# Optimization experiments

Measured on AMD Instinct MI355X. Metric: run time of the kernel, lower is better.

The kernel has to match this reference:

```python
import jax, jax.numpy as jnp
import numpy as np

HEADS = 16
DIM_HEAD = 64
WINDOW = 128
LOOK_BACKWARD = 1
LOOK_FORWARD = 0
THETA = 10000.0
PAD_VALUE = -1


def look_around(x, backward, forward, pad_value, axis):
    """Gather overlapping windows: concat shifted copies along the intra-window axis."""
    w = x.shape[axis]
    size = backward + forward + 1
    pads = [(0, 0)] * x.ndim
    pads[axis] = (backward, forward)
    p = jnp.pad(x, pads, constant_values=pad_value)
    segs = [jax.lax.slice_in_dim(p, s, s + w, axis=axis) for s in range(size)]
    return jnp.concatenate(segs, axis=axis + 1)


def rotate_half(t):
    t1, t2 = jnp.split(t, 2, axis=-1)
    return jnp.concatenate([-t2, t1], axis=-1)


def setup_inputs() -> dict:
    key = jax.random.key(0)
    k1, k2, k3 = jax.random.split(key, 3)
    dim = 1024
    x = jax.random.normal(k1, (4, 4096, dim), dtype=jnp.float32)
    W_qkv = jax.random.normal(k2, (dim, 3 * HEADS * DIM_HEAD), dtype=jnp.float32) * (dim ** -0.5)
    W_out = jax.random.normal(k3, (HEADS * DIM_HEAD, dim), dtype=jnp.float32) * ((HEADS * DIM_HEAD) ** -0.5)
    return {"x": x, "W_qkv": W_qkv, "W_out": W_out}


def reference(x, W_qkv, W_out):
    b, n, dim = x.shape
    h, dh, ws = HEADS, DIM_HEAD, WINDOW
    w = n // ws
    j = ws * (LOOK_BACKWARD + LOOK_FORWARD + 1)  # 256 keys per query window

    qkv = x @ W_qkv  # (b, n, 3*h*dh)
    q, k, v = jnp.split(qkv, 3, axis=-1)

    def to_bhwnd(t):
        return t.reshape(b, n, h, dh).transpose(0, 2, 1, 3).reshape(b, h, w, ws, dh)

    bq = to_bhwnd(q) * (dh ** -0.5)
    bk = look_around(to_bhwnd(k), LOOK_BACKWARD, LOOK_FORWARD, float(PAD_VALUE), axis=2)
    bv = look_around(to_bhwnd(v), LOOK_BACKWARD, LOOK_FORWARD, float(PAD_VALUE), axis=2)

    # rotary embeddings over the look-around key length; queries use last ws positions
    inv_freq = 1.0 / (THETA ** (jnp.arange(0, dh, 2, dtype=jnp.float32) / dh))
    t_pos = jnp.arange(j, dtype=jnp.float32)
    freqs = t_pos[:, None] * inv_freq[None, :]
    freqs = jnp.concatenate([freqs, freqs], axis=-1)  # (j, dh)
    q_freqs = freqs[-ws:]
    bq = bq * jnp.cos(q_freqs) + rotate_half(bq) * jnp.sin(q_freqs)
    bk = bk * jnp.cos(freqs) + rotate_half(bk) * jnp.sin(freqs)

    sim = jnp.einsum('bhwid,bhwjd->bhwij', bq, bk)  # (b,h,w,ws,j)

    seq = jnp.arange(n).reshape(w, ws)
    bq_t = seq[:, :, None]  # (w, ws, 1)
    bq_k = look_around(seq[None], LOOK_BACKWARD, LOOK_FORWARD, PAD_VALUE, axis=1)[0]  # (w, j)
    bq_k = bq_k[:, None, :]  # (w, 1, j)
    pad_mask = bq_k == PAD_VALUE
    # causal + exact window (look_backward * window_size)
    causal_mask = (bq_t < bq_k) | (bq_t > bq_k + ws * LOOK_BACKWARD)
    mask = causal_mask | pad_mask

    mask_value = -jnp.finfo(sim.dtype).max
    sim = jnp.where(mask, mask_value, sim)
    attn = jax.nn.softmax(sim, axis=-1)

    out = jnp.einsum('bhwij,bhwjd->bhwid', attn, bv)
    out = out.reshape(b, h, n, dh).transpose(0, 2, 1, 3).reshape(b, n, h * dh)
    return out @ W_out
```

## Files before the change

kernel.cpp:

```cpp
#include <hip/hip_runtime.h>
#include <stdint.h>


typedef __attribute__((ext_vector_type(8))) short bfrag;
typedef __attribute__((ext_vector_type(4))) float f4;

#define MFMA_BF16(a, b, c) __builtin_amdgcn_mfma_f32_16x16x32_bf16((a), (b), (c), 0, 0, 0)

static __device__ __forceinline__ short f2bf(float f) {
  unsigned u = __builtin_bit_cast(unsigned, f);
  u = (u + 0x7fffu + ((u >> 16) & 1u)) >> 16;
  return (short)u;
}
static __device__ __forceinline__ float bf2f(short s) {
  unsigned u = ((unsigned)(unsigned short)s) << 16;
  return __builtin_bit_cast(float, u);
}

typedef __attribute__((address_space(3))) unsigned lds_u;
typedef __attribute__((address_space(1))) unsigned gbl_u;

static __device__ __forceinline__ void gl_lds16(const void* g, const void* lds) {
  unsigned loff = (unsigned)__builtin_amdgcn_readfirstlane((int)(uintptr_t)lds);
  __builtin_amdgcn_global_load_lds((gbl_u*)(uintptr_t)g, (lds_u*)(uintptr_t)loff, 16, 0, 0);
}

__global__ __launch_bounds__(256) void convert_x(const float* __restrict__ x,
                                                 short* __restrict__ xb) {
  int idx = blockIdx.x * 256 + threadIdx.x;
  size_t base = (size_t)idx * 8;
  float4 a = *(const float4*)(x + base);
  float4 b = *(const float4*)(x + base + 4);
  bfrag o;
  o[0] = f2bf(a.x); o[1] = f2bf(a.y); o[2] = f2bf(a.z); o[3] = f2bf(a.w);
  o[4] = f2bf(b.x); o[5] = f2bf(b.y); o[6] = f2bf(b.z); o[7] = f2bf(b.w);
  *(bfrag*)(xb + base) = o;
}

__global__ __launch_bounds__(256) void transpose_w(
    const float* __restrict__ wqkv, const float* __restrict__ wout,
    short* __restrict__ wqkvT, short* __restrict__ woutT) {
  __shared__ short t[64][72];
  const int tid = threadIdx.x;
  const int kt = blockIdx.x, yt = blockIdx.y;
  const float* src; short* dst; int N, nt;
  if (yt < 48) { src = wqkv; dst = wqkvT; N = 3072; nt = yt; }
  else         { src = wout; dst = woutT; N = 1024; nt = yt - 48; }
  const int k0 = kt * 64, n0 = nt * 64;
#pragma unroll
  for (int i = 0; i < 4; ++i) {
    int r = i * 16 + (tid >> 4);
    int c = (tid & 15) * 4;
    float4 v = *(const float4*)(src + (size_t)(k0 + r) * N + n0 + c);
    t[c + 0][r] = f2bf(v.x);
    t[c + 1][r] = f2bf(v.y);
    t[c + 2][r] = f2bf(v.z);
    t[c + 3][r] = f2bf(v.w);
  }
  __syncthreads();
#pragma unroll
  for (int i = 0; i < 2; ++i) {
    int c = tid + i * 256;
    int n = c >> 3, k8 = (c & 7) * 8;
    *(bfrag*)(dst + (size_t)(n0 + n) * 1024 + k0 + k8) = *(const bfrag*)&t[n][k8];
  }
}

#define VM4 asm volatile("s_waitcnt vmcnt(4)" ::: "memory")
#define VM0 asm volatile("s_waitcnt vmcnt(0)" ::: "memory")
#define VNOP ((void)0)

#define ST_A(buf, ks, kk)                                                          \
  do {                                                                             \
    gl_lds16(aS0 + (kk), ldsA + (buf) * 32768 + (ks) * 16384 + stA);               \
    gl_lds16(aS1 + (kk), ldsA + (buf) * 32768 + (ks) * 16384 + 8192 + stA);        \
  } while (0)
#define ST_B(buf, ks, kk)                                                          \
  do {                                                                             \
    gl_lds16(bS0 + (kk), ldsB + (buf) * 32768 + (ks) * 16384 + stA);               \
    gl_lds16(bS1 + (kk), ldsB + (buf) * 32768 + (ks) * 16384 + 8192 + stA);        \
  } while (0)
#define ST2(buf, ks, kk) do { ST_A(buf, ks, kk); ST_B(buf, ks, kk); } while (0)

#define MM4(R, mi)                                            \
  acc[mi][0] = MFMA_BF16(fa[mi], fb[R][0], acc[mi][0]);       \
  acc[mi][1] = MFMA_BF16(fa[mi], fb[R][1], acc[mi][1]);       \
  acc[mi][2] = MFMA_BF16(fa[mi], fb[R][2], acc[mi][2]);       \
  acc[mi][3] = MFMA_BF16(fa[mi], fb[R][3], acc[mi][3])

#define SGB_M4 __builtin_amdgcn_sched_group_barrier(0x8, 4, 0)
#define SGB_D1 __builtin_amdgcn_sched_group_barrier(0x100, 1, 0)
#define SGB_D4 __builtin_amdgcn_sched_group_barrier(0x100, 4, 0)

#define PH(R, S, nbuf, nks, STAGE, WAIT)                                           \
  {                                                                                \
    const char* nA_ = ldsA + (nbuf) * 32768 + (nks) * 16384 + aRd;                 \
    const char* nB_ = ldsB + (nbuf) * 32768 + (nks) * 16384 + bRd;                 \
    asm volatile("s_waitcnt lgkmcnt(0)" ::: "memory");                             \
    __builtin_amdgcn_sched_barrier(0);                                             \
    __builtin_amdgcn_s_setprio(1);                                                 \
    MM4(R, 0); fa[0] = *(const bfrag*)(nA_);                                       \
    MM4(R, 1); fa[1] = *(const bfrag*)(nA_ + 1024);                                \
    MM4(R, 2); fa[2] = *(const bfrag*)(nA_ + 2048);                                \
    MM4(R, 3); fa[3] = *(const bfrag*)(nA_ + 3072);                                \
    MM4(R, 4); fa[4] = *(const bfrag*)(nA_ + 4096);                                \
    MM4(R, 5); fa[5] = *(const bfrag*)(nA_ + 5120);                                \
    MM4(R, 6); fa[6] = *(const bfrag*)(nA_ + 6144);                                \
    MM4(R, 7); fa[7] = *(const bfrag*)(nA_ + 7168);                                \
    fb[S][0] = *(const bfrag*)(nB_);                                               \
    fb[S][1] = *(const bfrag*)(nB_ + 1024);                                        \
    fb[S][2] = *(const bfrag*)(nB_ + 2048);                                        \
    fb[S][3] = *(const bfrag*)(nB_ + 3072);                                        \
    SGB_M4; SGB_D1; SGB_M4; SGB_D1; SGB_M4; SGB_D1; SGB_M4; SGB_D1;                \
    SGB_M4; SGB_D1; SGB_M4; SGB_D1; SGB_M4; SGB_D1; SGB_M4; SGB_D1;                \
    SGB_D4;                                                                        \
    __builtin_amdgcn_s_setprio(0);                                                 \
    STAGE;                                                                         \
    WAIT;                                                                          \
    __builtin_amdgcn_s_barrier();                                                  \
  }

#define PH_LAST(R)                                                                 \
  {                                                                                \
    asm volatile("s_waitcnt lgkmcnt(0)" ::: "memory");                             \
    __builtin_amdgcn_sched_barrier(0);                                             \
    __builtin_amdgcn_s_setprio(1);                                                 \
    MM4(R, 0); MM4(R, 1); MM4(R, 2); MM4(R, 3);                                    \
    MM4(R, 4); MM4(R, 5); MM4(R, 6); MM4(R, 7);                                    \
    __builtin_amdgcn_s_setprio(0);                                                 \
  }

template <int MODE, int NBX>
__global__ __launch_bounds__(512, 1) void gemm256(
    const short* __restrict__ A, const short* __restrict__ Bt, float* __restrict__ C,
    short* __restrict__ oq, short* __restrict__ ok, short* __restrict__ ov) {
  __shared__ __align__(1024) char lds[131072];
  char* const ldsA = lds;
  char* const ldsB = lds + 65536;

  const int tid = threadIdx.x, lane = tid & 63, wv = tid >> 6;
  const int wr = wv >> 2, wc = wv & 3;
  const int l15 = lane & 15, quad = lane >> 4;

  const int nwg = NBX * 64;
  const int bid = (int)blockIdx.x;
  const int wgid = (bid & 7) * (nwg >> 3) + (bid >> 3);
  const int bx = wgid % NBX, by = wgid / NBX;

  const short* Ab = A + (size_t)by * 256 * 1024;
  const short* Bb = Bt + (size_t)bx * 256 * 1024;

  const int srow = lane & 15, scg = lane >> 4;
  const short* aS0 = Ab + (size_t)(wv * 16 + srow) * 1024 + scg * 8;
  const short* aS1 = Ab + (size_t)((8 + wv) * 16 + srow) * 1024 + scg * 8;
  const short* bS0 = Bb + (size_t)(wv * 16 + srow) * 1024 + scg * 8;
  const short* bS1 = Bb + (size_t)((8 + wv) * 16 + srow) * 1024 + scg * 8;
  const int stA = wv * 1024;

  const int aRd = wr * 8192 + lane * 16;
  const int bRd = wc * 4096 + lane * 16;

  f4 acc[8][4];
#pragma unroll
  for (int i = 0; i < 8; ++i)
#pragma unroll
    for (int j = 0; j < 4; ++j) acc[i][j] = (f4)0.f;

  bfrag fa[8];
  bfrag fb[2][4];

  ST2(0, 0, 0); ST2(0, 1, 32); ST2(1, 0, 64);
  VM4;
  __builtin_amdgcn_s_barrier();
  {
    const char* pA0 = ldsA + aRd;
    const char* pB0 = ldsB + bRd;
    fa[0] = *(const bfrag*)(pA0);
    fa[1] = *(const bfrag*)(pA0 + 1024);
    fa[2] = *(const bfrag*)(pA0 + 2048);
    fa[3] = *(const bfrag*)(pA0 + 3072);
    fa[4] = *(const bfrag*)(pA0 + 4096);
    fa[5] = *(const bfrag*)(pA0 + 5120);
    fa[6] = *(const bfrag*)(pA0 + 6144);
    fa[7] = *(const bfrag*)(pA0 + 7168);
    fb[0][0] = *(const bfrag*)(pB0);
    fb[0][1] = *(const bfrag*)(pB0 + 1024);
    fb[0][2] = *(const bfrag*)(pB0 + 2048);
    fb[0][3] = *(const bfrag*)(pB0 + 3072);
  }

#pragma unroll 1
  for (int i = 0; i < 7; ++i) {
    const int k3 = i * 128 + 96, k4 = i * 128 + 128;
    const int k5 = i * 128 + 160, k6 = i * 128 + 192;
    PH(0, 1, 0, 1, ST2(1, 1, k3), VM4);
    PH(1, 0, 1, 0, ST2(0, 0, k4), VM4);
    PH(0, 1, 1, 1, ST2(0, 1, k5), VM4);
    PH(1, 0, 0, 0, ST2(1, 0, k6), VM4);
  }

  PH(0, 1, 0, 1, ST2(1, 1, 992), VM4);
  PH(1, 0, 1, 0, VNOP, VM0);
  PH(0, 1, 1, 1, VNOP, VNOP);
  PH_LAST(1);

  if constexpr (MODE == 0) {
    const int n64 = bx * 256 + wc * 64;
    const int part = n64 >> 10;
    const int head = (n64 & 1023) >> 6;
    short* o = (part == 0) ? oq : (part == 1) ? ok : ov;
    const int mbase = by * 256 + wr * 128;
    const int bb = mbase >> 12;
    const int p0 = (mbase & 4095) + quad * 4;
    short* const obase = o + (size_t)(bb * 16 + head) * 4096 * 64;
    if (part == 2) {
#pragma unroll
      for (int i = 0; i < 8; ++i)
#pragma unroll
        for (int r = 0; r < 4; ++r) {
          short* row = obase + (size_t)(p0 + i * 16 + r) * 64;
#pragma unroll
          for (int j = 0; j < 4; ++j) row[j * 16 + l15] = f2bf(acc[i][j][r]);
        }
    } else {
      const float qs = (part == 0) ? 0.125f : 1.0f;
      float fr[2], c1[2], s1[2], cD[2], sD[2], cs[2], sn[2];
      fr[0] = exp2f((float)l15 * -0.41524101186f);
      fr[1] = exp2f((float)(16 + l15) * -0.41524101186f);
#pragma unroll
      for (int j = 0; j < 2; ++j) {
        __sincosf(fr[j], &s1[j], &c1[j]);
        __sincosf(13.0f * fr[j], &sD[j], &cD[j]);
        __sincosf((float)p0 * fr[j], &sn[j], &cs[j]);
      }
#pragma unroll
      for (int i = 0; i < 8; ++i) {
#pragma unroll
        for (int r = 0; r < 4; ++r) {
          short* row = obase + (size_t)(p0 + i * 16 + r) * 64;
#pragma unroll
          for (int j = 0; j < 2; ++j) {
            float av = acc[i][j][r], bv2 = acc[i][j + 2][r];
            float ra = (av * cs[j] - bv2 * sn[j]) * qs;
            float rb = (bv2 * cs[j] + av * sn[j]) * qs;
            row[j * 16 + l15] = f2bf(ra);
            row[32 + j * 16 + l15] = f2bf(rb);
          }
          if (r < 3) {
#pragma unroll
            for (int j = 0; j < 2; ++j) {
              float nc = cs[j] * c1[j] - sn[j] * s1[j];
              sn[j] = sn[j] * c1[j] + cs[j] * s1[j];
              cs[j] = nc;
            }
          }
        }
#pragma unroll
        for (int j = 0; j < 2; ++j) {
          float nc = cs[j] * cD[j] - sn[j] * sD[j];
          sn[j] = sn[j] * cD[j] + cs[j] * sD[j];
          cs[j] = nc;
        }
      }
    }
  } else {
#pragma unroll
    for (int i = 0; i < 8; ++i)
#pragma unroll
      for (int j = 0; j < 4; ++j)
#pragma unroll
        for (int r = 0; r < 4; ++r) {
          int m = by * 256 + wr * 128 + i * 16 + quad * 4 + r;
          int n = bx * 256 + wc * 64 + j * 16 + l15;
          C[(size_t)m * 1024 + n] = acc[i][j][r];
        }
  }
}

__global__ __launch_bounds__(256) void attn_kernel(
    const short* __restrict__ qb, const short* __restrict__ kb,
    const short* __restrict__ vb, short* __restrict__ ob) {
  constexpr int KST = 72, VST = 264, PST = 136;
  __shared__ __align__(16) short smem[18432 + 16896];
  short* Ks = smem;
  short* Pl = smem;
  short* Vt = smem + 18432;

  const int bid = blockIdx.x;
  const int w = bid & 31, bh = bid >> 5;
  const int tid = threadIdx.x, lane = tid & 63, wv = tid >> 6;
  const int l15 = lane & 15, quad = lane >> 4;
  const size_t kvbase = (size_t)bh * (4096 * 64);
  const int pk0 = w * 128 - 128;

  const int i0 = wv * 32;
  const short* qbase = qb + kvbase + (size_t)(w * 128) * 64;
  bfrag aq[2][2];
#pragma unroll
  for (int rt = 0; rt < 2; ++rt)
#pragma unroll
    for (int ks = 0; ks < 2; ++ks)
      aq[rt][ks] = *(const bfrag*)(qbase + (size_t)(i0 + rt * 16 + l15) * 64 + ks * 32 + quad * 8);

#pragma unroll
  for (int i = 0; i < 8; ++i) {
    int c = tid + i * 256;
    int row = c >> 3;
    int d0 = (c & 7) * 8;
    int pk = pk0 + row;
    if (pk < 0) pk = 0;
    const size_t src = kvbase + (size_t)pk * 64 + d0;
    bfrag kvv = *(const bfrag*)(kb + src);
    *(bfrag*)&Ks[row * KST + d0] = kvv;
    bfrag vvv = *(const bfrag*)(vb + src);
#pragma unroll
    for (int j = 0; j < 8; ++j) Vt[(d0 + j) * VST + row] = vvv[j];
  }
  __syncthreads();

  f4 sim[2][16];
#pragma unroll
  for (int rt = 0; rt < 2; ++rt)
#pragma unroll
    for (int ct = 0; ct < 16; ++ct) sim[rt][ct] = (f4)0.f;

#pragma unroll
  for (int ct = 0; ct < 16; ++ct) {
    bfrag bk0 = *(const bfrag*)&Ks[(ct * 16 + l15) * KST + quad * 8];
    bfrag bk1 = *(const bfrag*)&Ks[(ct * 16 + l15) * KST + 32 + quad * 8];
#pragma unroll
    for (int rt = 0; rt < 2; ++rt) {
      sim[rt][ct] = MFMA_BF16(aq[rt][0], bk0, sim[rt][ct]);
      sim[rt][ct] = MFMA_BF16(aq[rt][1], bk1, sim[rt][ct]);
    }
  }
  __syncthreads();

  float linv[2][4];
#pragma unroll
  for (int rt = 0; rt < 2; ++rt)
#pragma unroll
    for (int r = 0; r < 4; ++r) {
      const int iloc = i0 + rt * 16 + quad * 4 + r;
      float sum = 0.f;
#pragma unroll
      for (int ct = 0; ct < 16; ++ct) {
        int jj = ct * 16 + l15;
        bool valid = (jj >= iloc) && (jj <= iloc + 128) && ((w > 0) || (jj >= 128));
        float pv = valid ? __expf(sim[rt][ct][r]) : 0.f;
        sim[rt][ct][r] = pv;
        sum += pv;
      }
#pragma unroll
      for (int off = 1; off < 16; off <<= 1) sum += __shfl_xor(sum, off);
      linv[rt][r] = 1.f / sum;
    }

  f4 oacc[2][4];
#pragma unroll
  for (int rt = 0; rt < 2; ++rt)
#pragma unroll
    for (int ctd = 0; ctd < 4; ++ctd) oacc[rt][ctd] = (f4)0.f;

#pragma unroll
  for (int pass = 0; pass < 2; ++pass) {
#pragma unroll
    for (int rt = 0; rt < 2; ++rt)
#pragma unroll
      for (int ct = 0; ct < 8; ++ct) {
        int ctg = pass * 8 + ct;
#pragma unroll
        for (int r = 0; r < 4; ++r)
          Pl[(i0 + rt * 16 + quad * 4 + r) * PST + ct * 16 + l15] = f2bf(sim[rt][ctg][r]);
      }
#pragma unroll
    for (int ks = 0; ks < 4; ++ks) {
      bfrag ap[2];
#pragma unroll
      for (int rt = 0; rt < 2; ++rt)
        ap[rt] = *(const bfrag*)&Pl[(i0 + rt * 16 + l15) * PST + ks * 32 + quad * 8];
#pragma unroll
      for (int ctd = 0; ctd < 4; ++ctd) {
        bfrag bv = *(const bfrag*)&Vt[(ctd * 16 + l15) * VST + pass * 128 + ks * 32 + quad * 8];
#pragma unroll
        for (int rt = 0; rt < 2; ++rt) oacc[rt][ctd] = MFMA_BF16(ap[rt], bv, oacc[rt][ctd]);
      }
    }
  }

  const int b = bh >> 4, h = bh & 15;
  short* obase = ob + ((size_t)b * 4096 + w * 128) * 1024 + h * 64;
#pragma unroll
  for (int rt = 0; rt < 2; ++rt)
#pragma unroll
    for (int ctd = 0; ctd < 4; ++ctd)
#pragma unroll
      for (int r = 0; r < 4; ++r) {
        int i = i0 + rt * 16 + quad * 4 + r;
        int d = ctd * 16 + l15;
        obase[(size_t)i * 1024 + d] = f2bf(oacc[rt][ctd][r] * linv[rt][r]);
      }
}

extern "C" void kernel_launch(void* const* d_in, const int* in_sizes, int n_in,
                              void* d_out, int out_size, void* d_ws, size_t ws_size,
                              hipStream_t stream) {
  const float* x = (const float*)d_in[0];
  const float* wqkv = (const float*)d_in[1];
  const float* wout = (const float*)d_in[2];
  float* out = (float*)d_out;
  char* ws = (char*)d_ws;

  short* qb = (short*)(ws + 0);
  short* kb = (short*)(ws + 33554432);
  short* vb = (short*)(ws + 67108864);
  short* xb = (short*)(ws + 100663296);
  short* ab = xb;
  short* wqkvT = (short*)(ws + 134217728);
  short* woutT = (short*)(ws + 140509184);

  convert_x<<<8192, 256, 0, stream>>>(x, xb);
  transpose_w<<<dim3(16, 64), 256, 0, stream>>>(wqkv, wout, wqkvT, woutT);
  gemm256<0, 12><<<768, 512, 0, stream>>>(xb, wqkvT, nullptr, qb, kb, vb);
  attn_kernel<<<2048, 256, 0, stream>>>(qb, kb, vb, ab);
  gemm256<1, 4><<<256, 512, 0, stream>>>(ab, woutT, out, nullptr, nullptr, nullptr);
}
```

Measured before the change: 363.8 us.

## Swap MFMA operands to transpose accumulators and vectorize epilogue stores

Swaps the A and B operands of every MFMA in the GEMM and attention kernels so each lane's accumulator holds four consecutive columns of a single row instead of four rows. The epilogues then pack and store bf16 pairs as 8-byte vectors and fp32 results as 16-byte vectors, replacing scalar 2- and 4-byte stores. The softmax row sum now needs only two cross-lane shuffles. The rotary recurrence is reworked to step by 16 positions with per-column frequencies, which adds more sincos setup per lane.

```diff
diff --git a/kernel.cpp b/kernel.cpp
--- a/kernel.cpp
+++ b/kernel.cpp
@@ -4,6 +4,7 @@
 
 typedef __attribute__((ext_vector_type(8))) short bfrag;
 typedef __attribute__((ext_vector_type(4))) float f4;
+typedef __attribute__((ext_vector_type(2))) unsigned u32x2;
 
 #define MFMA_BF16(a, b, c) __builtin_amdgcn_mfma_f32_16x16x32_bf16((a), (b), (c), 0, 0, 0)
 
@@ -12,9 +13,8 @@
   u = (u + 0x7fffu + ((u >> 16) & 1u)) >> 16;
   return (short)u;
 }
-static __device__ __forceinline__ float bf2f(short s) {
-  unsigned u = ((unsigned)(unsigned short)s) << 16;
-  return __builtin_bit_cast(float, u);
+static __device__ __forceinline__ unsigned pack2(float a, float b) {
+  return (unsigned)(unsigned short)f2bf(a) | ((unsigned)(unsigned short)f2bf(b) << 16);
 }
 
 typedef __attribute__((address_space(3))) unsigned lds_u;
@@ -83,10 +83,10 @@
 #define ST2(buf, ks, kk) do { ST_A(buf, ks, kk); ST_B(buf, ks, kk); } while (0)
 
 #define MM4(R, mi)                                            \
-  acc[mi][0] = MFMA_BF16(fa[mi], fb[R][0], acc[mi][0]);       \
-  acc[mi][1] = MFMA_BF16(fa[mi], fb[R][1], acc[mi][1]);       \
-  acc[mi][2] = MFMA_BF16(fa[mi], fb[R][2], acc[mi][2]);       \
-  acc[mi][3] = MFMA_BF16(fa[mi], fb[R][3], acc[mi][3])
+  acc[mi][0] = MFMA_BF16(fb[R][0], fa[mi], acc[mi][0]);       \
+  acc[mi][1] = MFMA_BF16(fb[R][1], fa[mi], acc[mi][1]);       \
+  acc[mi][2] = MFMA_BF16(fb[R][2], fa[mi], acc[mi][2]);       \
+  acc[mi][3] = MFMA_BF16(fb[R][3], fa[mi], acc[mi][3])
 
 #define SGB_M4 __builtin_amdgcn_sched_group_barrier(0x8, 4, 0)
 #define SGB_D1 __builtin_amdgcn_sched_group_barrier(0x100, 1, 0)
@@ -198,7 +198,6 @@
     PH(0, 1, 1, 1, ST2(0, 1, k5), VM4);
     PH(1, 0, 0, 0, ST2(1, 0, k6), VM4);
   }
-
   PH(0, 1, 0, 1, ST2(1, 1, 992), VM4);
   PH(1, 0, 1, 0, VNOP, VM0);
   PH(0, 1, 1, 1, VNOP, VNOP);
@@ -211,69 +210,67 @@
     short* o = (part == 0) ? oq : (part == 1) ? ok : ov;
     const int mbase = by * 256 + wr * 128;
     const int bb = mbase >> 12;
-    const int p0 = (mbase & 4095) + quad * 4;
+    const int pl = (mbase & 4095) + l15;
     short* const obase = o + (size_t)(bb * 16 + head) * 4096 * 64;
     if (part == 2) {
 #pragma unroll
-      for (int i = 0; i < 8; ++i)
-#pragma unroll
-        for (int r = 0; r < 4; ++r) {
-          short* row = obase + (size_t)(p0 + i * 16 + r) * 64;
-#pragma unroll
-          for (int j = 0; j < 4; ++j) row[j * 16 + l15] = f2bf(acc[i][j][r]);
+      for (int mi = 0; mi < 8; ++mi) {
+        short* row = obase + (size_t)(pl + mi * 16) * 64;
+#pragma unroll
+        for (int j = 0; j < 4; ++j) {
+          u32x2 pk; pk[0] = pack2(acc[mi][j][0], acc[mi][j][1]);
+          pk[1] = pack2(acc[mi][j][2], acc[mi][j][3]);
+          *(u32x2*)(row + j * 16 + quad * 4) = pk;
         }
+      }
     } else {
       const float qs = (part == 0) ? 0.125f : 1.0f;
-      float fr[2], c1[2], s1[2], cD[2], sD[2], cs[2], sn[2];
-      fr[0] = exp2f((float)l15 * -0.41524101186f);
-      fr[1] = exp2f((float)(16 + l15) * -0.41524101186f);
-#pragma unroll
-      for (int j = 0; j < 2; ++j) {
-        __sincosf(fr[j], &s1[j], &c1[j]);
-        __sincosf(13.0f * fr[j], &sD[j], &cD[j]);
-        __sincosf((float)p0 * fr[j], &sn[j], &cs[j]);
-      }
-#pragma unroll
-      for (int i = 0; i < 8; ++i) {
+      float fr[2][4], cs[2][4], sn[2][4], c16[2][4], s16[2][4];
+#pragma unroll
+      for (int j = 0; j < 2; ++j)
 #pragma unroll
         for (int r = 0; r < 4; ++r) {
-          short* row = obase + (size_t)(p0 + i * 16 + r) * 64;
-#pragma unroll
-          for (int j = 0; j < 2; ++j) {
-            float av = acc[i][j][r], bv2 = acc[i][j + 2][r];
-            float ra = (av * cs[j] - bv2 * sn[j]) * qs;
-            float rb = (bv2 * cs[j] + av * sn[j]) * qs;
-            row[j * 16 + l15] = f2bf(ra);
-            row[32 + j * 16 + l15] = f2bf(rb);
+          fr[j][r] = exp2f((float)(j * 16 + quad * 4 + r) * -0.41524101186f);
+          __sincosf((float)pl * fr[j][r], &sn[j][r], &cs[j][r]);
+          __sincosf(16.0f * fr[j][r], &s16[j][r], &c16[j][r]);
+        }
+#pragma unroll
+      for (int mi = 0; mi < 8; ++mi) {
+        short* row = obase + (size_t)(pl + mi * 16) * 64;
+#pragma unroll
+        for (int j = 0; j < 2; ++j) {
+          float ra[4], rb[4];
+#pragma unroll
+          for (int r = 0; r < 4; ++r) {
+            float av = acc[mi][j][r], bv2 = acc[mi][j + 2][r];
+            ra[r] = (av * cs[j][r] - bv2 * sn[j][r]) * qs;
+            rb[r] = (bv2 * cs[j][r] + av * sn[j][r]) * qs;
           }
-          if (r < 3) {
-#pragma unroll
-            for (int j = 0; j < 2; ++j) {
-              float nc = cs[j] * c1[j] - sn[j] * s1[j];
-              sn[j] = sn[j] * c1[j] + cs[j] * s1[j];
-              cs[j] = nc;
+          u32x2 pa; pa[0] = pack2(ra[0], ra[1]); pa[1] = pack2(ra[2], ra[3]);
+          u32x2 pb; pb[0] = pack2(rb[0], rb[1]); pb[1] = pack2(rb[2], rb[3]);
+          *(u32x2*)(row + j * 16 + quad * 4) = pa;
+          *(u32x2*)(row + 32 + j * 16 + quad * 4) = pb;
+        }
+        if (mi < 7) {
+#pragma unroll
+          for (int j = 0; j < 2; ++j)
+#pragma unroll
+            for (int r = 0; r < 4; ++r) {
+              float nc = cs[j][r] * c16[j][r] - sn[j][r] * s16[j][r];
+              sn[j][r] = sn[j][r] * c16[j][r] + cs[j][r] * s16[j][r];
+              cs[j][r] = nc;
             }
-          }
-        }
-#pragma unroll
-        for (int j = 0; j < 2; ++j) {
-          float nc = cs[j] * cD[j] - sn[j] * sD[j];
-          sn[j] = sn[j] * cD[j] + cs[j] * sD[j];
-          cs[j] = nc;
         }
       }
     }
   } else {
-#pragma unroll
-    for (int i = 0; i < 8; ++i)
+    const int m0 = by * 256 + wr * 128 + l15;
+    const int n0 = bx * 256 + wc * 64 + quad * 4;
+#pragma unroll
+    for (int mi = 0; mi < 8; ++mi)
 #pragma unroll
       for (int j = 0; j < 4; ++j)
-#pragma unroll
-        for (int r = 0; r < 4; ++r) {
-          int m = by * 256 + wr * 128 + i * 16 + quad * 4 + r;
-          int n = bx * 256 + wc * 64 + j * 16 + l15;
-          C[(size_t)m * 1024 + n] = acc[i][j][r];
-        }
+        *(f4*)(C + (size_t)(m0 + mi * 16) * 1024 + n0 + j * 16) = acc[mi][j];
   }
 }
 
@@ -330,31 +327,31 @@
     bfrag bk1 = *(const bfrag*)&Ks[(ct * 16 + l15) * KST + 32 + quad * 8];
 #pragma unroll
     for (int rt = 0; rt < 2; ++rt) {
-      sim[rt][ct] = MFMA_BF16(aq[rt][0], bk0, sim[rt][ct]);
-      sim[rt][ct] = MFMA_BF16(aq[rt][1], bk1, sim[rt][ct]);
+      sim[rt][ct] = MFMA_BF16(bk0, aq[rt][0], sim[rt][ct]);
+      sim[rt][ct] = MFMA_BF16(bk1, aq[rt][1], sim[rt][ct]);
     }
   }
   __syncthreads();
 
-  float linv[2][4];
-#pragma unroll
-  for (int rt = 0; rt < 2; ++rt)
-#pragma unroll
-    for (int r = 0; r < 4; ++r) {
-      const int iloc = i0 + rt * 16 + quad * 4 + r;
-      float sum = 0.f;
-#pragma unroll
-      for (int ct = 0; ct < 16; ++ct) {
-        int jj = ct * 16 + l15;
+  float linv[2];
+#pragma unroll
+  for (int rt = 0; rt < 2; ++rt) {
+    const int iloc = i0 + rt * 16 + l15;
+    float sum = 0.f;
+#pragma unroll
+    for (int ct = 0; ct < 16; ++ct)
+#pragma unroll
+      for (int r = 0; r < 4; ++r) {
+        int jj = ct * 16 + quad * 4 + r;
         bool valid = (jj >= iloc) && (jj <= iloc + 128) && ((w > 0) || (jj >= 128));
         float pv = valid ? __expf(sim[rt][ct][r]) : 0.f;
         sim[rt][ct][r] = pv;
         sum += pv;
       }
-#pragma unroll
-      for (int off = 1; off < 16; off <<= 1) sum += __shfl_xor(sum, off);
-      linv[rt][r] = 1.f / sum;
-    }
+    sum += __shfl_xor(sum, 16);
+    sum += __shfl_xor(sum, 32);
+    linv[rt] = 1.f / sum;
+  }
 
   f4 oacc[2][4];
 #pragma unroll
@@ -369,9 +366,10 @@
 #pragma unroll
       for (int ct = 0; ct < 8; ++ct) {
         int ctg = pass * 8 + ct;
-#pragma unroll
-        for (int r = 0; r < 4; ++r)
-          Pl[(i0 + rt * 16 + quad * 4 + r) * PST + ct * 16 + l15] = f2bf(sim[rt][ctg][r]);
+        u32x2 pk;
+        pk[0] = pack2(sim[rt][ctg][0], sim[rt][ctg][1]);
+        pk[1] = pack2(sim[rt][ctg][2], sim[rt][ctg][3]);
+        *(u32x2*)&Pl[(i0 + rt * 16 + l15) * PST + ct * 16 + quad * 4] = pk;
       }
 #pragma unroll
     for (int ks = 0; ks < 4; ++ks) {
@@ -383,7 +381,8 @@
       for (int ctd = 0; ctd < 4; ++ctd) {
         bfrag bv = *(const bfrag*)&Vt[(ctd * 16 + l15) * VST + pass * 128 + ks * 32 + quad * 8];
 #pragma unroll
-        for (int rt = 0; rt < 2; ++rt) oacc[rt][ctd] = MFMA_BF16(ap[rt], bv, oacc[rt][ctd]);
+        for (int rt = 0; rt < 2; ++rt)
+          oacc[rt][ctd] = MFMA_BF16(bv, ap[rt], oacc[rt][ctd]);
       }
     }
   }
@@ -391,15 +390,16 @@
   const int b = bh >> 4, h = bh & 15;
   short* obase = ob + ((size_t)b * 4096 + w * 128) * 1024 + h * 64;
 #pragma unroll
-  for (int rt = 0; rt < 2; ++rt)
-#pragma unroll
-    for (int ctd = 0; ctd < 4; ++ctd)
-#pragma unroll
-      for (int r = 0; r < 4; ++r) {
-        int i = i0 + rt * 16 + quad * 4 + r;
-        int d = ctd * 16 + l15;
-        obase[(size_t)i * 1024 + d] = f2bf(oacc[rt][ctd][r] * linv[rt][r]);
-      }
+  for (int rt = 0; rt < 2; ++rt) {
+    const int q = i0 + rt * 16 + l15;
+#pragma unroll
+    for (int ctd = 0; ctd < 4; ++ctd) {
+      u32x2 pk;
+      pk[0] = pack2(oacc[rt][ctd][0] * linv[rt], oacc[rt][ctd][1] * linv[rt]);
+      pk[1] = pack2(oacc[rt][ctd][2] * linv[rt], oacc[rt][ctd][3] * linv[rt]);
+      *(u32x2*)(obase + (size_t)q * 1024 + ctd * 16 + quad * 4) = pk;
+    }
+  }
 }
 
 extern "C" void kernel_launch(void* const* d_in, const int* in_sizes, int n_in,
```

New measurement: 372.1 us. 1.02x slower.
